# Kernel tuning notes

Measured on AMD Instinct MI355X. Metric: run time of the kernel, lower is better.

Reference implementation:

```python
import jax, jax.numpy as jnp
import numpy as np

IN_CH = 1280
NUM_HEADS = 8
DIM_DOWN = 5
CUT_RATE = 4
SCALE = (IN_CH // NUM_HEADS) ** -0.5  # faithful to original: uses in_ch//num_heads


def setup_inputs() -> dict:
    key = jax.random.key(0)
    ks = jax.random.split(key, 5)
    B, N = 4, 4096
    C = IN_CH // DIM_DOWN  # 256
    x = jax.random.normal(ks[0], (B, N, IN_CH), dtype=jnp.float32)
    Wd = jax.random.normal(ks[1], (IN_CH, C), dtype=jnp.float32) * (IN_CH ** -0.5)
    Wqkv = jax.random.normal(ks[2], (C, 3 * C), dtype=jnp.float32) * (C ** -0.5)
    Wup = jax.random.normal(ks[3], (C, IN_CH), dtype=jnp.float32) * (C ** -0.5)
    bup = jnp.zeros((IN_CH,), dtype=jnp.float32)
    return {"x": x, "Wd": Wd, "Wqkv": Wqkv, "Wup": Wup, "bup": bup}


def reference(x, Wd, Wqkv, Wup, bup):
    # dim-down projection (dropout is identity at rate 0 / eval)
    h = x @ Wd                                  # [B, N, C]
    B, N, C = h.shape
    H = NUM_HEADS
    hd = C // H
    blk = N // CUT_RATE
    qkv = (h @ Wqkv).reshape(B, N, 3, H, hd)
    qkv = jnp.transpose(qkv, (2, 0, 3, 1, 4))   # [3, B, H, N, hd]
    q, k, v = qkv[0], qkv[1], qkv[2]
    # block-diagonal local attention: split N into CUT_RATE independent chunks
    q = q.reshape(B, H, CUT_RATE, blk, hd)
    k = k.reshape(B, H, CUT_RATE, blk, hd)
    v = v.reshape(B, H, CUT_RATE, blk, hd)
    attn = jnp.einsum('bhcqd,bhckd->bhcqk', q, k) * SCALE
    attn = jax.nn.softmax(attn, axis=-1)
    o = jnp.einsum('bhcqk,bhckd->bhcqd', attn, v)
    # torch cat over chunks along token dim, then merge heads: [B, N, C]
    o = jnp.transpose(o, (0, 2, 3, 1, 4)).reshape(B, N, C)
    return o @ Wup + bup
```

## Files before the change

### kernel.cpp

```cpp
#include <hip/hip_runtime.h>

typedef unsigned short u16;
typedef unsigned int u32;
typedef u16 u16x8 __attribute__((ext_vector_type(8)));
typedef __bf16 bf16x8 __attribute__((ext_vector_type(8)));
typedef float f32x4 __attribute__((ext_vector_type(4)));

__device__ __forceinline__ u16 f2bf(float f) {
  union { float f; unsigned u; } c; c.f = f;
  unsigned u = c.u;
  return (u16)((u + 0x7fff + ((u >> 16) & 1)) >> 16);
}

__device__ __forceinline__ float fexp2(float x) {
  float r; asm("v_exp_f32 %0, %1" : "=v"(r) : "v"(x)); return r;
}

__device__ __forceinline__ u32 cvtpk(float lo, float hi) {
  u32 r;
  asm("v_cvt_pk_bf16_f32 %0, %1, %2" : "=v"(r) : "v"(lo), "v"(hi));
  return r;
}

__device__ __forceinline__ void lds16(const u16* g, u16* l) {
  __builtin_amdgcn_global_load_lds(
      (const __attribute__((address_space(1))) unsigned int*)g,
      (__attribute__((address_space(3))) unsigned int*)l, 16, 0, 0);
}

#define CEXP (0.07905694150420949f * 1.4426950408889634f)

#define PREP_W (1280 * 256 + 768 * 256 + 1280 * 256)

__global__ __launch_bounds__(256)
void prep_all(const float* __restrict__ Wd, const float* __restrict__ Wqkv,
              const float* __restrict__ Wup, const float* __restrict__ X,
              u16* __restrict__ WdC, u16* __restrict__ WqkvT,
              u16* __restrict__ WupT, u16* __restrict__ Xb, int n8) {
  int id = blockIdx.x * 256 + threadIdx.x;
  if (id < 1280 * 256) {
    WdC[id] = f2bf(Wd[id]);
    return;
  }
  id -= 1280 * 256;
  if (id < 768 * 256) {
    int n = id >> 8, c = id & 255;
    float v = Wqkv[(size_t)c * 768 + n];
    if (n < 256) v *= CEXP;
    WqkvT[id] = f2bf(v);
    return;
  }
  id -= 768 * 256;
  if (id < 1280 * 256) {
    int n = id >> 8, c = id & 255;
    WupT[id] = f2bf(Wup[(size_t)c * 1280 + n]);
    return;
  }
  id -= 1280 * 256;
  if (id < n8) {
    const float4* src = (const float4*)(X + (size_t)id * 8);
    float4 lo = src[0], hi = src[1];
    u16x8 v;
    v[0]=f2bf(lo.x); v[1]=f2bf(lo.y); v[2]=f2bf(lo.z); v[3]=f2bf(lo.w);
    v[4]=f2bf(hi.x); v[5]=f2bf(hi.y); v[6]=f2bf(hi.z); v[7]=f2bf(hi.w);
    *(u16x8*)(Xb + (size_t)id * 8) = v;
  }
}

template <int AF32>
__global__ __launch_bounds__(256)
void gemm_bt(const void* __restrict__ Av,
             const u16* __restrict__ BT,
             u16* __restrict__ Cb, float* __restrict__ Cf,
             const float* __restrict__ bias,
             int M, int N, int K)
{
  __shared__ u16 As[128][64];
  __shared__ u16 Bs[128][64];
  const int tid  = threadIdx.x;
  const int wave = tid >> 6, lane = tid & 63;
  const int quad = lane >> 4, l16 = lane & 15;
  const int rsw  = l16 & 7;
  const int ssw  = ((lane & 7) ^ (lane >> 3)) << 3;

  const int nb = N >> 7, mb = M >> 7;
  int band, nblk;
  if ((mb & 7) == 0) {
    int xcd = blockIdx.x & 7, slot = blockIdx.x >> 3;
    band = xcd + 8 * (slot / nb);
    nblk = slot % nb;
  } else {
    band = blockIdx.x / nb;
    nblk = blockIdx.x % nb;
  }
  const int m0 = band * 128, n0 = nblk * 128;
  const int wr = (wave >> 1) * 64, wc = (wave & 1) * 64;
  const u16*   A16 = (const u16*)Av;
  const float* A32 = (const float*)Av;

  f32x4 acc[4][4];
#pragma unroll
  for (int i = 0; i < 4; i++)
#pragma unroll
    for (int j = 0; j < 4; j++) acc[i][j] = f32x4{0.f, 0.f, 0.f, 0.f};

  for (int k0 = 0; k0 < K; k0 += 64) {
    if constexpr (AF32) {
#pragma unroll
      for (int it = 0; it < 4; it++) {
        int idx = tid + it * 256;
        int r = idx >> 3;
        const float* src = &A32[(size_t)(m0 + r) * K + k0 + ((idx & 7) << 3)];
        float4 lo = *(const float4*)src;
        float4 hi = *(const float4*)(src + 4);
        u16x8 v;
        v[0]=f2bf(lo.x); v[1]=f2bf(lo.y); v[2]=f2bf(lo.z); v[3]=f2bf(lo.w);
        v[4]=f2bf(hi.x); v[5]=f2bf(hi.y); v[6]=f2bf(hi.z); v[7]=f2bf(hi.w);
        *(u16x8*)&As[r][((idx & 7) ^ (r & 7)) << 3] = v;
      }
#pragma unroll
      for (int it = 0; it < 4; it++) {
        int r0 = wave * 32 + it * 8;
        lds16(&BT[(size_t)(n0 + r0 + (lane >> 3)) * K + k0 + ssw],
              &Bs[r0][0] + lane * 8);
      }
    } else {
#pragma unroll
      for (int it = 0; it < 4; it++) {
        int r0 = wave * 32 + it * 8;
        lds16(&A16[(size_t)(m0 + r0 + (lane >> 3)) * K + k0 + ssw],
              &As[r0][0] + lane * 8);
        lds16(&BT[(size_t)(n0 + r0 + (lane >> 3)) * K + k0 + ssw],
              &Bs[r0][0] + lane * 8);
      }
    }
    __syncthreads();
#pragma unroll
    for (int ks = 0; ks < 64; ks += 32) {
      bf16x8 af[4], bfr[4];
#pragma unroll
      for (int i = 0; i < 4; i++)
        af[i] = *(const bf16x8*)&As[wr + i * 16 + l16][(((ks >> 3) + quad) ^ rsw) << 3];
#pragma unroll
      for (int j = 0; j < 4; j++)
        bfr[j] = *(const bf16x8*)&Bs[wc + j * 16 + l16][(((ks >> 3) + quad) ^ rsw) << 3];
#pragma unroll
      for (int i = 0; i < 4; i++)
#pragma unroll
        for (int j = 0; j < 4; j++)
          acc[i][j] = __builtin_amdgcn_mfma_f32_16x16x32_bf16(af[i], bfr[j], acc[i][j], 0, 0, 0);
    }
    __syncthreads();
  }

#pragma unroll
  for (int i = 0; i < 4; i++) {
#pragma unroll
    for (int j = 0; j < 4; j++) {
      int col = n0 + wc + j * 16 + l16;
      float bv = bias ? bias[col] : 0.0f;
#pragma unroll
      for (int r = 0; r < 4; r++) {
        int row = m0 + wr + i * 16 + quad * 4 + r;
        float v = acc[i][j][r] + bv;
        if (Cf) Cf[(size_t)row * N + col] = v;
        else    Cb[(size_t)row * N + col] = f2bf(v);
      }
    }
  }
}

#define BAR()  do { asm volatile("" ::: "memory"); \
                    __builtin_amdgcn_s_barrier(); \
                    asm volatile("" ::: "memory"); } while (0)
#define VMC(n) asm volatile("s_waitcnt vmcnt(" #n ")" ::: "memory")

#define LDA_(d, ib) { _Pragma("unroll") for (int i = 0; i < 4; i++) \
  _Pragma("unroll") for (int ks = 0; ks < 2; ks++) \
    af[i*2+ks] = *(const bf16x8*)&As[d][wm][(ib+i)*16 + l16][((ks*4+quad) ^ rsw) << 3]; }

#define LDB_(d, dst, jp) { _Pragma("unroll") for (int j = 0; j < 2; j++) \
  _Pragma("unroll") for (int ks = 0; ks < 2; ks++) \
    dst[j*2+ks] = *(const bf16x8*)&Bs[d][bh][br + (jp*2+j)*16 + l16][((ks*4+quad) ^ rsw) << 3]; }

#define MM_(ib, jp, breg) { __builtin_amdgcn_s_setprio(1); \
  _Pragma("unroll") for (int i = 0; i < 4; i++) \
  _Pragma("unroll") for (int j = 0; j < 2; j++) \
  _Pragma("unroll") for (int ks = 0; ks < 2; ks++) \
    acc[ib+i][jp*2+j] = __builtin_amdgcn_mfma_f32_16x16x32_bf16( \
        af[i*2+ks], breg[j*2+ks], acc[ib+i][jp*2+j], 0, 0, 0); \
  __builtin_amdgcn_s_setprio(0); }

__global__ __launch_bounds__(512, 2)
void gemm_bt256(const u16* __restrict__ A16, const u16* __restrict__ BT,
                u16* __restrict__ Cb, int M, int N, int K)
{
  __shared__ __align__(16) u16 As[2][2][128][64];
  __shared__ __align__(16) u16 Bs[2][2][128][64];
  const int tid  = threadIdx.x;
  const int wave = tid >> 6, lane = tid & 63;
  const int quad = lane >> 4, l16 = lane & 15;
  const int wm = wave >> 2, wn = wave & 3;
  const int bh = wn >> 1, br = (wn & 1) * 64;
  const int rsw = l16 & 7;

  const int nb = N >> 8, mb = M >> 8;
  int band, nblk;
  if ((mb & 7) == 0) {
    int xcd = blockIdx.x & 7, slot = blockIdx.x >> 3;
    band = xcd + 8 * (slot / nb);
    nblk = slot % nb;
  } else {
    band = blockIdx.x / nb;
    nblk = blockIdx.x % nb;
  }
  const int m0 = band * 256, n0 = nblk * 256;
  const int NT = K >> 6;

  const int srow = tid >> 3;
  const int scol = ((tid & 7) ^ (srow & 7)) << 3;

  auto stageA = [&](int t, int h) {
    const int d = t & 1;
    const size_t g = (size_t)(m0 + h * 128 + srow) * K + (t << 6) + scol;
    lds16(&A16[g], &As[d][h][0][0] + tid * 8);
    lds16(&A16[g + (size_t)64 * K], &As[d][h][64][0] + tid * 8);
  };
  auto stageB = [&](int t, int h) {
    const int d = t & 1;
    const size_t g = (size_t)(n0 + h * 128 + srow) * K + (t << 6) + scol;
    lds16(&BT[g], &Bs[d][h][0][0] + tid * 8);
    lds16(&BT[g + (size_t)64 * K], &Bs[d][h][64][0] + tid * 8);
  };

  bf16x8 af[8], b0[4], b1[4];
  f32x4 acc[8][4];
#pragma unroll
  for (int i = 0; i < 8; i++)
#pragma unroll
    for (int j = 0; j < 4; j++) acc[i][j] = f32x4{0.f, 0.f, 0.f, 0.f};

  stageA(0, 0); stageA(0, 1); stageB(0, 0); stageB(0, 1); stageA(1, 0);
  VMC(2);
  BAR();

  const int nIter = NT >> 1;
  for (int it = 0; it < nIter; ++it) {
    const int t0 = it * 2, t1 = t0 + 1;
    const bool more  = (t0 + 2 < NT);
    const bool more1 = (t1 + 2 < NT);

    LDA_(0, 0); LDB_(0, b0, 0);
    stageA(t1, 1);
    BAR(); MM_(0, 0, b0); BAR();
    LDB_(0, b1, 1);
    stageB(t1, 0);
    BAR(); MM_(0, 1, b1); BAR();
    LDA_(0, 4);
    stageB(t1, 1);
    BAR(); MM_(4, 1, b1); BAR();
    if (more) stageA(t0 + 2, 0);
    BAR(); MM_(4, 0, b0);
    if (more) { VMC(2); } else { VMC(0); }
    BAR();

    LDA_(1, 0); LDB_(1, b0, 0);
    if (more) stageA(t0 + 2, 1);
    BAR(); MM_(0, 0, b0); BAR();
    LDB_(1, b1, 1);
    if (more) stageB(t0 + 2, 0);
    BAR(); MM_(0, 1, b1); BAR();
    LDA_(1, 4);
    if (more) stageB(t0 + 2, 1);
    BAR(); MM_(4, 1, b1); BAR();
    if (more1) stageA(t1 + 2, 0);
    BAR(); MM_(4, 0, b0);
    if (it + 1 < nIter) {
      if (more1) { VMC(2); } else { VMC(0); }
      BAR();
    }
  }

#pragma unroll
  for (int i = 0; i < 8; i++) {
#pragma unroll
    for (int j = 0; j < 4; j++) {
      const int col = n0 + wn * 64 + j * 16 + l16;
#pragma unroll
      for (int r = 0; r < 4; r++) {
        const int row = m0 + wm * 128 + i * 16 + quad * 4 + r;
        Cb[(size_t)row * N + col] = f2bf(acc[i][j][r]);
      }
    }
  }
}

__global__ __launch_bounds__(256)
void vtrans(const u16* __restrict__ qkv, u16* __restrict__ vT)
{
  __shared__ u16 T[32][72];
  const int tid   = threadIdx.x;
  const int kt    = blockIdx.x;
  const int head  = blockIdx.y >> 2;
  const int chunk = blockIdx.y & 3;
  const int b     = blockIdx.z;
  const size_t rowbase = (size_t)b * 4096 + chunk * 1024 + kt * 64;

  const int tok = tid >> 2;
  const int d8  = (tid & 3) << 3;
  u16x8 vv = *(const u16x8*)&qkv[(rowbase + tok) * 768 + 512 + head * 32 + d8];
  const int rot = (tok + (d8 >> 3)) & 7;
#pragma unroll
  for (int jj = 0; jj < 8; jj++) {
    int j = (jj + rot) & 7;
    T[d8 + j][tok] = vv[j];
  }
  __syncthreads();
  const int d = tid >> 3;
  const int s = tid & 7;
  u16x8 out = *(const u16x8*)&T[d][s * 8];
  size_t obase = ((size_t)((b * 4 + chunk) * 8 + head)) * 32768
               + (size_t)d * 1024 + kt * 64 + s * 8;
  *(u16x8*)&vT[obase] = out;
}

__global__ __launch_bounds__(256)
void attn_kernel(const u16* __restrict__ qkv, const u16* __restrict__ vT,
                 u16* __restrict__ o)
{
  __shared__ __align__(16) u16 Ks[2][64][32];
  __shared__ __align__(16) u16 VTs[2][32][64];
  __shared__ u16 Ps[4][32][72];

  const int tid  = threadIdx.x;
  const int wave = tid >> 6, lane = tid & 63;
  const int quad = lane >> 4, l16 = lane & 15;
  const int qb    = blockIdx.x;
  const int head  = blockIdx.y >> 2;
  const int chunk = blockIdx.y & 3;
  const int b     = blockIdx.z;
  const size_t rowbase = (size_t)b * 4096 + chunk * 1024;
  const int tok0 = qb * 128 + wave * 32;

  const int kkey = tid >> 2;
  const int kd8  = (tid & 3) << 3;
  const int vr   = tid >> 3;
  const int vs   = tid & 7;
  const int vsl  = (vs ^ (vr & 7)) << 3;
  const size_t vbase = ((size_t)((b * 4 + chunk) * 8 + head)) * 32768
                     + (size_t)vr * 1024 + vsl;

  auto stageKV = [&](int kb, int buf) {
    lds16(&qkv[(rowbase + kb * 64 + kkey) * 768 + 256 + head * 32 + kd8],
          &Ks[buf][0][0] + tid * 8);
    lds16(&vT[vbase + (size_t)kb * 64], &VTs[buf][0][0] + tid * 8);
  };

  stageKV(0, 0);

  bf16x8 qf[2];
#pragma unroll
  for (int qt = 0; qt < 2; qt++)
    qf[qt] = *(const bf16x8*)&qkv[(rowbase + tok0 + qt * 16 + l16) * 768 + head * 32 + quad * 8];

  float lsum[2] = {0.f, 0.f};
  f32x4 Oacc[2][2];
#pragma unroll
  for (int qt = 0; qt < 2; qt++)
#pragma unroll
    for (int nd = 0; nd < 2; nd++) Oacc[qt][nd] = f32x4{0.f, 0.f, 0.f, 0.f};

  __syncthreads();

  for (int kb = 0; kb < 16; kb++) {
    const int cur = kb & 1;
    if (kb < 15) stageKV(kb + 1, cur ^ 1);

    bf16x8 kf[4];
#pragma unroll
    for (int kt = 0; kt < 4; kt++)
      kf[kt] = *(const bf16x8*)&Ks[cur][kt * 16 + l16][quad * 8];

    f32x4 ST[4][2];
    __builtin_amdgcn_s_setprio(1);
#pragma unroll
    for (int kt = 0; kt < 4; kt++)
#pragma unroll
      for (int qt = 0; qt < 2; qt++)
        ST[kt][qt] = __builtin_amdgcn_mfma_f32_16x16x32_bf16(kf[kt], qf[qt], f32x4{0.f,0.f,0.f,0.f}, 0, 0, 0);
    __builtin_amdgcn_s_setprio(0);

#pragma unroll
    for (int qt = 0; qt < 2; qt++) {
#pragma unroll
      for (int kt = 0; kt < 4; kt++) {
        float p0 = fexp2(ST[kt][qt][0]);
        float p1 = fexp2(ST[kt][qt][1]);
        float p2 = fexp2(ST[kt][qt][2]);
        float p3 = fexp2(ST[kt][qt][3]);
        lsum[qt] += (p0 + p1) + (p2 + p3);
        uint2 dd;
        dd.x = cvtpk(p0, p1);
        dd.y = cvtpk(p2, p3);
        *(uint2*)&Ps[wave][qt * 16 + l16][kt * 16 + quad * 4] = dd;
      }
    }

#pragma unroll
    for (int ks = 0; ks < 2; ks++) {
      bf16x8 vf[2], pf[2];
#pragma unroll
      for (int nd = 0; nd < 2; nd++)
        vf[nd] = *(const bf16x8*)&VTs[cur][nd * 16 + l16][((ks * 4 + quad) ^ (l16 & 7)) << 3];
#pragma unroll
      for (int qt = 0; qt < 2; qt++)
        pf[qt] = *(const bf16x8*)&Ps[wave][qt * 16 + l16][ks * 32 + quad * 8];
      __builtin_amdgcn_s_setprio(1);
#pragma unroll
      for (int qt = 0; qt < 2; qt++)
#pragma unroll
        for (int nd = 0; nd < 2; nd++)
          Oacc[qt][nd] = __builtin_amdgcn_mfma_f32_16x16x32_bf16(pf[qt], vf[nd], Oacc[qt][nd], 0, 0, 0);
      __builtin_amdgcn_s_setprio(0);
    }

    __syncthreads();
  }

#pragma unroll
  for (int qt = 0; qt < 2; qt++) {
    float s = lsum[qt];
    s += __shfl_xor(s, 16);
    s += __shfl_xor(s, 32);
    lsum[qt] = s;
  }
#pragma unroll
  for (int qt = 0; qt < 2; qt++)
#pragma unroll
    for (int r = 0; r < 4; r++) {
      float inv = 1.0f / __shfl(lsum[qt], quad * 4 + r, 16);
      size_t row = rowbase + tok0 + qt * 16 + quad * 4 + r;
#pragma unroll
      for (int nd = 0; nd < 2; nd++) {
        int col = head * 32 + nd * 16 + l16;
        o[row * 256 + col] = f2bf(Oacc[qt][nd][r] * inv);
      }
    }
}

extern "C" void kernel_launch(void* const* d_in, const int* in_sizes, int n_in,
                              void* d_out, int out_size, void* d_ws, size_t ws_size,
                              hipStream_t stream)
{
  const float* x    = (const float*)d_in[0];
  const float* Wd   = (const float*)d_in[1];
  const float* Wqkv = (const float*)d_in[2];
  const float* Wup  = (const float*)d_in[3];
  const float* bup  = (const float*)d_in[4];
  float* out = (float*)d_out;

  const int M = 4 * 4096;

  u16* WdC   = (u16*)d_ws;
  u16* WqkvT = WdC   + 1280 * 256;
  u16* WupT  = WqkvT + 768 * 256;
  u16* WpT   = WupT  + 1280 * 256;
  u16* qkv   = WpT   + 768 * 1280;
  u16* ob    = qkv   + (size_t)M * 768;
  u16* xb    = ob    + (size_t)M * 256;
  u16* vT    = xb;

  const size_t need = ((size_t)(1280*256 + 768*256 + 1280*256 + 768*1280)
                       + (size_t)M * (768 + 256 + 1280)) * sizeof(u16);
  const bool use_xb = ws_size >= need;

  const int n8 = use_xb ? (M * 1280 / 8) : 0;
  prep_all<<<(PREP_W + n8 + 255) / 256, 256, 0, stream>>>(
      Wd, Wqkv, Wup, x, WdC, WqkvT, WupT, xb, n8);

  gemm_bt<0><<<dim3((1280 / 128) * (768 / 128)), 256, 0, stream>>>(
      (const void*)WqkvT, WdC, WpT, nullptr, nullptr, 768, 1280, 256);

  if (use_xb) {
    gemm_bt256<<<dim3((768 / 256) * (M / 256)), 512, 0, stream>>>(
        xb, WpT, qkv, M, 768, 1280);
  } else {
    gemm_bt<1><<<dim3((768 / 128) * (M / 128)), 256, 0, stream>>>(
        (const void*)x, WpT, qkv, nullptr, nullptr, M, 768, 1280);
  }

  vtrans<<<dim3(16, 32, 4), 256, 0, stream>>>(qkv, vT);

  attn_kernel<<<dim3(8, 32, 4), 256, 0, stream>>>(qkv, vT, ob);

  gemm_bt<0><<<dim3((1280 / 128) * (M / 128)), 256, 0, stream>>>(
      (const void*)ob, WupT, nullptr, out, bup, M, 1280, 256);
}
```

Before: 277.5 us.

## Keep P in registers, deepen attention KV prefetch, use 256-tile GEMM for up-projection

The attention kernel now packs softmax probabilities into registers and feeds them straight into the PV MFMA instead of round-tripping through LDS. It also widens K/V staging to four buffers with a prefetch distance of two, waiting on vmcnt with raw barriers instead of __syncthreads. The final up-projection switches to the 256x256 gemm_bt256 kernel, templated to write fp32 output with bias. The vtrans readout pattern changes so the V-transpose layout matches the register-resident P fragment ordering. These aim to cut LDS traffic, hide load latency, and speed the output GEMM, at the cost of more LDS per block and possible occupancy or register pressure.

```diff
diff --git a/kernel.cpp b/kernel.cpp
--- a/kernel.cpp
+++ b/kernel.cpp
@@ -2,6 +2,7 @@
 
 typedef unsigned short u16;
 typedef unsigned int u32;
+typedef u16 u16x4 __attribute__((ext_vector_type(4)));
 typedef u16 u16x8 __attribute__((ext_vector_type(8)));
 typedef __bf16 bf16x8 __attribute__((ext_vector_type(8)));
 typedef float f32x4 __attribute__((ext_vector_type(4)));
@@ -29,6 +30,11 @@
 }
 
 #define CEXP (0.07905694150420949f * 1.4426950408889634f)
+
+#define BAR()  do { asm volatile("" ::: "memory"); \
+                    __builtin_amdgcn_s_barrier(); \
+                    asm volatile("" ::: "memory"); } while (0)
+#define VMC(n) asm volatile("s_waitcnt vmcnt(" #n ")" ::: "memory")
 
 #define PREP_W (1280 * 256 + 768 * 256 + 1280 * 256)
 
@@ -170,11 +176,6 @@
   }
 }
 
-#define BAR()  do { asm volatile("" ::: "memory"); \
-                    __builtin_amdgcn_s_barrier(); \
-                    asm volatile("" ::: "memory"); } while (0)
-#define VMC(n) asm volatile("s_waitcnt vmcnt(" #n ")" ::: "memory")
-
 #define LDA_(d, ib) { _Pragma("unroll") for (int i = 0; i < 4; i++) \
   _Pragma("unroll") for (int ks = 0; ks < 2; ks++) \
     af[i*2+ks] = *(const bf16x8*)&As[d][wm][(ib+i)*16 + l16][((ks*4+quad) ^ rsw) << 3]; }
@@ -191,9 +192,11 @@
         af[i*2+ks], breg[j*2+ks], acc[ib+i][jp*2+j], 0, 0, 0); \
   __builtin_amdgcn_s_setprio(0); }
 
+template <int F32OUT>
 __global__ __launch_bounds__(512, 2)
 void gemm_bt256(const u16* __restrict__ A16, const u16* __restrict__ BT,
-                u16* __restrict__ Cb, int M, int N, int K)
+                u16* __restrict__ Cb, float* __restrict__ Cf,
+                const float* __restrict__ bias, int M, int N, int K)
 {
   __shared__ __align__(16) u16 As[2][2][128][64];
   __shared__ __align__(16) u16 Bs[2][2][128][64];
@@ -286,10 +289,12 @@
 #pragma unroll
     for (int j = 0; j < 4; j++) {
       const int col = n0 + wn * 64 + j * 16 + l16;
+      float bv = F32OUT ? bias[col] : 0.0f;
 #pragma unroll
       for (int r = 0; r < 4; r++) {
         const int row = m0 + wm * 128 + i * 16 + quad * 4 + r;
-        Cb[(size_t)row * N + col] = f2bf(acc[i][j][r]);
+        if constexpr (F32OUT) Cf[(size_t)row * N + col] = acc[i][j][r] + bv;
+        else                  Cb[(size_t)row * N + col] = f2bf(acc[i][j][r]);
       }
     }
   }
@@ -318,19 +323,23 @@
   __syncthreads();
   const int d = tid >> 3;
   const int s = tid & 7;
-  u16x8 out = *(const u16x8*)&T[d][s * 8];
+  const int base = ((s >> 2) << 5) + ((s & 3) << 2);
+  u16x4 lo = *(const u16x4*)&T[d][base];
+  u16x4 hi = *(const u16x4*)&T[d][base + 16];
+  u16x8 o8;
+  o8[0]=lo[0]; o8[1]=lo[1]; o8[2]=lo[2]; o8[3]=lo[3];
+  o8[4]=hi[0]; o8[5]=hi[1]; o8[6]=hi[2]; o8[7]=hi[3];
   size_t obase = ((size_t)((b * 4 + chunk) * 8 + head)) * 32768
                + (size_t)d * 1024 + kt * 64 + s * 8;
-  *(u16x8*)&vT[obase] = out;
+  *(u16x8*)&vT[obase] = o8;
 }
 
 __global__ __launch_bounds__(256)
 void attn_kernel(const u16* __restrict__ qkv, const u16* __restrict__ vT,
                  u16* __restrict__ o)
 {
-  __shared__ __align__(16) u16 Ks[2][64][32];
-  __shared__ __align__(16) u16 VTs[2][32][64];
-  __shared__ u16 Ps[4][32][72];
+  __shared__ __align__(16) u16 Ks[4][64][32];
+  __shared__ __align__(16) u16 VTs[4][32][64];
 
   const int tid  = threadIdx.x;
   const int wave = tid >> 6, lane = tid & 63;
@@ -363,6 +372,8 @@
   for (int qt = 0; qt < 2; qt++)
     qf[qt] = *(const bf16x8*)&qkv[(rowbase + tok0 + qt * 16 + l16) * 768 + head * 32 + quad * 8];
 
+  stageKV(1, 1);
+
   float lsum[2] = {0.f, 0.f};
   f32x4 Oacc[2][2];
 #pragma unroll
@@ -370,11 +381,12 @@
 #pragma unroll
     for (int nd = 0; nd < 2; nd++) Oacc[qt][nd] = f32x4{0.f, 0.f, 0.f, 0.f};
 
-  __syncthreads();
+  VMC(2);
+  BAR();
 
   for (int kb = 0; kb < 16; kb++) {
-    const int cur = kb & 1;
-    if (kb < 15) stageKV(kb + 1, cur ^ 1);
+    const int cur = kb & 3;
+    if (kb + 2 < 16) stageKV(kb + 2, (kb + 2) & 3);
 
     bf16x8 kf[4];
 #pragma unroll
@@ -390,8 +402,9 @@
         ST[kt][qt] = __builtin_amdgcn_mfma_f32_16x16x32_bf16(kf[kt], qf[qt], f32x4{0.f,0.f,0.f,0.f}, 0, 0, 0);
     __builtin_amdgcn_s_setprio(0);
 
-#pragma unroll
-    for (int qt = 0; qt < 2; qt++) {
+    u32 pw[2][4][2];
+#pragma unroll
+    for (int qt = 0; qt < 2; qt++)
 #pragma unroll
       for (int kt = 0; kt < 4; kt++) {
         float p0 = fexp2(ST[kt][qt][0]);
@@ -399,32 +412,35 @@
         float p2 = fexp2(ST[kt][qt][2]);
         float p3 = fexp2(ST[kt][qt][3]);
         lsum[qt] += (p0 + p1) + (p2 + p3);
-        uint2 dd;
-        dd.x = cvtpk(p0, p1);
-        dd.y = cvtpk(p2, p3);
-        *(uint2*)&Ps[wave][qt * 16 + l16][kt * 16 + quad * 4] = dd;
-      }
-    }
+        pw[qt][kt][0] = cvtpk(p0, p1);
+        pw[qt][kt][1] = cvtpk(p2, p3);
+      }
 
 #pragma unroll
     for (int ks = 0; ks < 2; ks++) {
-      bf16x8 vf[2], pf[2];
+      bf16x8 vf[2];
 #pragma unroll
       for (int nd = 0; nd < 2; nd++)
         vf[nd] = *(const bf16x8*)&VTs[cur][nd * 16 + l16][((ks * 4 + quad) ^ (l16 & 7)) << 3];
-#pragma unroll
-      for (int qt = 0; qt < 2; qt++)
-        pf[qt] = *(const bf16x8*)&Ps[wave][qt * 16 + l16][ks * 32 + quad * 8];
       __builtin_amdgcn_s_setprio(1);
 #pragma unroll
-      for (int qt = 0; qt < 2; qt++)
+      for (int qt = 0; qt < 2; qt++) {
+        union { u32 w[4]; bf16x8 v; } pu;
+        pu.w[0] = pw[qt][2 * ks][0];
+        pu.w[1] = pw[qt][2 * ks][1];
+        pu.w[2] = pw[qt][2 * ks + 1][0];
+        pu.w[3] = pw[qt][2 * ks + 1][1];
 #pragma unroll
         for (int nd = 0; nd < 2; nd++)
-          Oacc[qt][nd] = __builtin_amdgcn_mfma_f32_16x16x32_bf16(pf[qt], vf[nd], Oacc[qt][nd], 0, 0, 0);
+          Oacc[qt][nd] = __builtin_amdgcn_mfma_f32_16x16x32_bf16(pu.v, vf[nd], Oacc[qt][nd], 0, 0, 0);
+      }
       __builtin_amdgcn_s_setprio(0);
     }
 
-    __syncthreads();
+    if (kb < 15) {
+      if (kb + 2 < 16) { VMC(2); } else { VMC(0); }
+      BAR();
+    }
   }
 
 #pragma unroll
@@ -482,8 +498,8 @@
       (const void*)WqkvT, WdC, WpT, nullptr, nullptr, 768, 1280, 256);
 
   if (use_xb) {
-    gemm_bt256<<<dim3((768 / 256) * (M / 256)), 512, 0, stream>>>(
-        xb, WpT, qkv, M, 768, 1280);
+    gemm_bt256<0><<<dim3((768 / 256) * (M / 256)), 512, 0, stream>>>(
+        xb, WpT, qkv, nullptr, nullptr, M, 768, 1280);
   } else {
     gemm_bt<1><<<dim3((768 / 128) * (M / 128)), 256, 0, stream>>>(
         (const void*)x, WpT, qkv, nullptr, nullptr, M, 768, 1280);
@@ -493,6 +509,6 @@
 
   attn_kernel<<<dim3(8, 32, 4), 256, 0, stream>>>(qkv, vT, ob);
 
-  gemm_bt<0><<<dim3((1280 / 128) * (M / 128)), 256, 0, stream>>>(
-      (const void*)ob, WupT, nullptr, out, bup, M, 1280, 256);
-}
+  gemm_bt256<1><<<dim3((1280 / 256) * (M / 256)), 512, 0, stream>>>(
+      ob, WupT, nullptr, out, bup, M, 1280, 256);
+}
```

Result: no change. 277.7 us (+0.1%).
